# Performance work log

Measured on AMD Instinct MI355X. Metric: run time of the kernel, lower is better.

## Reference

```python
import jax, jax.numpy as jnp
import numpy as np
import math

B, N, DMODEL, H = 8, 1024, 256, 8
HEAD_DIM = DMODEL // H


def setup_inputs() -> dict:
    key = jax.random.key(0)
    ks = jax.random.split(key, 8)
    x = jax.random.normal(ks[0], (B, N, DMODEL), dtype=jnp.float32)
    # symmetric-ish nonnegative pairwise distances
    adj = jax.random.uniform(ks[1], (B, N, N), dtype=jnp.float32) * 10.0
    mask = jax.random.uniform(ks[2], (B, N)) < 0.9  # bool, mostly valid nodes
    W_qkv = jax.random.normal(ks[3], (DMODEL, 3 * DMODEL), dtype=jnp.float32) / math.sqrt(DMODEL)
    b_qkv = jax.random.normal(ks[4], (3 * DMODEL,), dtype=jnp.float32) * 0.01
    shifts = jnp.arange(1.0, H + 1.0, dtype=jnp.float32)  # initial_shifts
    widths = jnp.ones((H,), dtype=jnp.float32)            # initial_widths
    # self_loop_W = 1/head_dim + U(0,1), non-trainable
    self_loop_w = 1.0 / HEAD_DIM + jax.random.uniform(ks[5], (H,), dtype=jnp.float32)
    return {"x": x, "adj": adj, "mask": mask, "W_qkv": W_qkv, "b_qkv": b_qkv,
            "shifts": shifts, "widths": widths, "self_loop_w": self_loop_w}


def reference(x, adj, mask, W_qkv, b_qkv, shifts, widths, self_loop_w):
    b, n, _ = x.shape
    h = shifts.shape[0]
    d = W_qkv.shape[1] // (3 * h)
    qkv = (x @ W_qkv + b_qkv).reshape(b, n, 3, h, d)
    qkv = jnp.transpose(qkv, (2, 0, 3, 1, 4))  # [3, B, H, N, D]
    Q, K, V = qkv[0], qkv[1], qkv[2]
    scores = jnp.einsum('bhnd,bhmd->bhnm', Q, K) / jnp.sqrt(jnp.float32(d))
    # Gaussian moire focus on adjacency distances, per head
    sh = shifts.reshape(1, h, 1, 1)
    w = jnp.maximum(widths, 0.5).reshape(1, h, 1, 1)
    moire = jnp.exp(-((adj[:, None, :, :] - sh) ** 2) / w)
    adjusted = scores + jnp.log(jnp.maximum(moire, 1e-6))
    eye = jnp.eye(n, dtype=adjusted.dtype)  # [N, N]
    adjusted = adjusted + eye * self_loop_w.reshape(1, h, 1, 1)
    mask2d = (mask[:, :, None] & mask[:, None, :])[:, None, :, :]  # [B,1,N,N]
    adjusted = jnp.where(mask2d, adjusted, jnp.float32(-1000000.0))
    attn = jax.nn.softmax(adjusted, axis=-1)
    out = jnp.einsum('bhnm,bhmd->bhnd', attn, V)
    return jnp.transpose(out, (0, 2, 1, 3)).reshape(b, n, h * d)
```

## Files before the change

### kernel.cpp

```cpp
#include <hip/hip_runtime.h>

#define BB 8
#define NN 1024
#define DM 256
#define HH 8
#define HD 32
#define TC 768

typedef __bf16 bf16x8 __attribute__((ext_vector_type(8)));
typedef __bf16 bf16x4 __attribute__((ext_vector_type(4)));
typedef float  f32x4  __attribute__((ext_vector_type(4)));
typedef unsigned int u32;

__global__ __launch_bounds__(256) void precast(
    const float* __restrict__ x, const float* __restrict__ W,
    __bf16* __restrict__ xb, __bf16* __restrict__ Wt)
{
  const int tid = threadIdx.x;
  const int bid = blockIdx.x;
  if (bid < 48) {
    __shared__ __bf16 T[64][65];
    const int ct = bid % 12, kt = bid / 12;
    const int c0 = ct * 64, k0 = kt * 64;
    #pragma unroll
    for (int i = 0; i < 16; ++i) {
      int e = tid + i * 256, kk = e >> 6, cc = e & 63;
      T[cc][kk] = (__bf16)W[(size_t)(k0 + kk) * TC + c0 + cc];
    }
    __syncthreads();
    #pragma unroll
    for (int i = 0; i < 16; ++i) {
      int e = tid + i * 256, cc = e >> 6, kk = e & 63;
      Wt[(size_t)(c0 + cc) * DM + k0 + kk] = T[cc][kk];
    }
  } else {
    const size_t e = (size_t)(bid - 48) * 256 + tid;
    const float4 v = ((const float4*)x)[e];
    bf16x4 o;
    o[0] = (__bf16)v.x; o[1] = (__bf16)v.y;
    o[2] = (__bf16)v.z; o[3] = (__bf16)v.w;
    ((bf16x4*)xb)[e] = o;
  }
}

__global__ __launch_bounds__(256, 3) void qkv_gemm(
    const __bf16* __restrict__ xb, const __bf16* __restrict__ Wt,
    const float* __restrict__ bias, __bf16* __restrict__ Qb,
    __bf16* __restrict__ Kb, __bf16* __restrict__ Vt)
{
  __shared__ __align__(16) char LDSU[49152];
  __bf16* As0 = (__bf16*)LDSU;
  __bf16* Bs0 = (__bf16*)(LDSU + 16384);
  __bf16* As1 = (__bf16*)(LDSU + 24576);
  __bf16* Bs1 = (__bf16*)(LDSU + 40960);

  const int tid  = threadIdx.x;
  const int w    = tid >> 6, lane = tid & 63;
  const int n16  = lane & 15, quad = lane >> 4;
  const int m0   = blockIdx.y * 128, c0 = blockIdx.x * 64;
  const int bb   = m0 >> 10, n0 = m0 & 1023;

  const int stRow = w*8 + (lane >> 3);
  const int stG   = (lane & 7) ^ (lane >> 3);
  const __bf16* gA = &xb[(size_t)(m0 + stRow)*DM + stG*8];
  const __bf16* gB = &Wt[(size_t)(c0 + stRow)*DM + stG*8];

#define QKV_STAGE(Adst, Bdst, K0) do {                                        \
    _Pragma("unroll")                                                         \
    for (int i_ = 0; i_ < 4; ++i_) {                                          \
      const __bf16* gp_ = gA + (size_t)(i_*32)*DM + (K0);                     \
      __bf16* lp_ = (Adst) + (i_*32 + w*8)*64;                                \
      __builtin_amdgcn_global_load_lds(                                       \
          (const __attribute__((address_space(1))) u32*)gp_,                  \
          (__attribute__((address_space(3))) u32*)lp_, 16, 0, 0);             \
    }                                                                         \
    _Pragma("unroll")                                                         \
    for (int i_ = 0; i_ < 2; ++i_) {                                          \
      const __bf16* gp_ = gB + (size_t)(i_*32)*DM + (K0);                     \
      __bf16* lp_ = (Bdst) + (i_*32 + w*8)*64;                                \
      __builtin_amdgcn_global_load_lds(                                       \
          (const __attribute__((address_space(1))) u32*)gp_,                  \
          (__attribute__((address_space(3))) u32*)lp_, 16, 0, 0);             \
    }                                                                         \
  } while (0)

  f32x4 acc[2][4] = {};

  QKV_STAGE(As0, Bs0, 0);
  __syncthreads();

  #pragma unroll
  for (int kk = 0; kk < 4; ++kk) {
    __bf16* Ac = (kk & 1) ? As1 : As0;
    __bf16* Bc = (kk & 1) ? Bs1 : Bs0;
    if (kk == 0)      QKV_STAGE(As1, Bs1, 64);
    else if (kk == 1) QKV_STAGE(As0, Bs0, 128);
    else if (kk == 2) QKV_STAGE(As1, Bs1, 192);
    #pragma unroll
    for (int ks = 0; ks < 2; ++ks) {
      const int ch = ((ks*4 + quad) ^ (n16 & 7)) * 8;
      bf16x8 af0 = *(const bf16x8*)&Ac[(w*32 + n16)*64 + ch];
      bf16x8 af1 = *(const bf16x8*)&Ac[(w*32 + 16 + n16)*64 + ch];
      #pragma unroll
      for (int cb = 0; cb < 4; ++cb) {
        bf16x8 bfb = *(const bf16x8*)&Bc[(cb*16 + n16)*64 + ch];
        acc[0][cb] = __builtin_amdgcn_mfma_f32_16x16x32_bf16(af0, bfb, acc[0][cb], 0, 0, 0);
        acc[1][cb] = __builtin_amdgcn_mfma_f32_16x16x32_bf16(af1, bfb, acc[1][cb], 0, 0, 0);
      }
    }
    __syncthreads();
  }

  float bv[4];
  #pragma unroll
  for (int cb = 0; cb < 4; ++cb) bv[cb] = bias[c0 + cb*16 + n16];

  if (c0 < 512) {
    __bf16* Ct = (__bf16*)LDSU;
    #pragma unroll
    for (int cb = 0; cb < 4; ++cb)
      #pragma unroll
      for (int mb = 0; mb < 2; ++mb)
        #pragma unroll
        for (int r = 0; r < 4; ++r)
          Ct[(w*32 + mb*16 + quad*4 + r)*72 + cb*16 + n16] =
              (__bf16)(acc[mb][cb][r] + bv[cb]);
    __syncthreads();
    const int chunk = tid & 3, hh = (tid >> 2) & 1, rbase = tid >> 3;
    const int c_head = c0 + hh*32;
    const int h = (c_head >> 5) & 7;
    __bf16* base = (c_head >> 8) ? Kb : Qb;
    #pragma unroll
    for (int it = 0; it < 4; ++it) {
      int rl = rbase + it*32;
      bf16x8 v = *(const bf16x8*)&Ct[rl*72 + hh*32 + chunk*8];
      *(bf16x8*)&base[((size_t)((bb*HH + h)*NN + n0 + rl))*HD + chunk*8] = v;
    }
  } else {
    __bf16* CtT = (__bf16*)LDSU;
    #pragma unroll
    for (int cb = 0; cb < 4; ++cb)
      #pragma unroll
      for (int mb = 0; mb < 2; ++mb) {
        bf16x4 t;
        #pragma unroll
        for (int r = 0; r < 4; ++r) t[r] = (__bf16)(acc[mb][cb][r] + bv[cb]);
        *(bf16x4*)&CtT[(cb*16 + n16)*136 + w*32 + mb*16 + quad*4] = t;
      }
    __syncthreads();
    const int col = tid >> 2, sg = tid & 3;
    const int c = c0 + col;
    const int h = (c >> 5) & 7, dd = c & 31;
    __bf16* dst = &Vt[((size_t)((bb*HH + h)*HD + dd))*NN + n0 + sg*32];
    const __bf16* srcp = &CtT[col*136 + sg*32];
    #pragma unroll
    for (int q2 = 0; q2 < 4; ++q2)
      *(bf16x8*)&dst[q2*8] = *(const bf16x8*)&srcp[q2*8];
  }
}

__global__ __launch_bounds__(256, 8) void attn_kernel(
    const __bf16* __restrict__ Q, const __bf16* __restrict__ K,
    const __bf16* __restrict__ Vt, const float* __restrict__ adj,
    const int* __restrict__ mask, const float* __restrict__ shifts,
    const float* __restrict__ widths, const float* __restrict__ slw,
    float* __restrict__ out)
{
  __shared__ __align__(16) __bf16 Ks[2][64][32];
  __shared__ __align__(16) __bf16 Vts[2][32][64];
  __shared__ __align__(16) __bf16 Ps[32][72];

  const int tid  = threadIdx.x;
  const int w    = tid >> 6, lane = tid & 63;
  const int n16  = lane & 15, quad = lane >> 4;
  const int qg   = w >> 1, jh = w & 1;
  const int bh   = blockIdx.x >> 5, qt = blockIdx.x & 31;
  const int b    = bh >> 3, h = bh & 7;
  const int q0   = qt * 32;

  const float L2E   = 1.4426950408889634f;
  const float sh    = shifts[h];
  const float ninvw = -L2E / fmaxf(widths[h], 0.5f);
  const float slv   = slw[h] * L2E;
  const float scl   = 0.17677669529663687f * L2E;
  const float MASKV = -28.0f;
  const float c1 = -2.0f * sh * ninvw;
  const float c2 = sh * sh * ninvw;

  const int srow = tid >> 2, sseg = tid & 3;
  const int vd   = tid >> 3, vsg  = tid & 7;
  const __bf16* Kg = K + (size_t)bh*NN*HD;
  const __bf16* Vg = Vt + (size_t)bh*HD*NN;
  const __bf16* ksrc = Kg + srow*HD + (sseg ^ (srow & 3))*8;
  const __bf16* vsrc = Vg + (size_t)vd*NN + (vsg ^ (vd & 7))*8;
  __bf16* kdst0 = &Ks[0][0][0] + tid*8;
  __bf16* kdst1 = &Ks[1][0][0] + tid*8;
  __bf16* vdst0 = &Vts[0][0][0] + tid*8;
  __bf16* vdst1 = &Vts[1][0][0] + tid*8;

#define GLDS(g, l) __builtin_amdgcn_global_load_lds(                          \
    (const __attribute__((address_space(1))) u32*)(g),                        \
    (__attribute__((address_space(3))) u32*)(l), 16, 0, 0)

  GLDS(ksrc, kdst0);
  GLDS(vsrc, vdst0);

  const bf16x8 qf =
      *(const bf16x8*)&Q[((size_t)bh*NN + q0 + qg*16 + n16)*HD + quad*8];
  int mq[4];
  #pragma unroll
  for (int r = 0; r < 4; ++r) mq[r] = mask[b*NN + q0 + qg*16 + quad*4 + r];

  const float* ar0 = adj + ((size_t)(b*NN + q0 + qg*16 + quad*4))*NN + jh*32 + n16;
  const float* ar1 = ar0 + NN;
  const float* ar2 = ar0 + 2*NN;
  const float* ar3 = ar0 + 3*NN;
  const int*   mrp = mask + b*NN + jh*32 + n16;

  const int kbc = (quad ^ (n16 & 3)) * 8;
  const int vbc = (((jh << 2) + quad) ^ (n16 & 7)) * 8;

  const f32x4 zero = {0.f, 0.f, 0.f, 0.f};
  f32x4 o0 = zero, o1 = zero, lacc = zero;
  bf16x8 onesb;
  #pragma unroll
  for (int i = 0; i < 8; ++i) onesb[i] = (__bf16)1.0f;

  const bool mydiagH = (jh == (qt & 1));
  const int  dT  = qt >> 1;
  const int  dlr = n16 - quad*4;

  __syncthreads();

  #pragma unroll 2
  for (int jtl = 0; jtl < 16; ++jtl) {
    const int cur = jtl & 1;
    const int j0  = jtl * 64;

    if (jtl < 15) {
      const __bf16* kg = ksrc + (size_t)(j0 + 64)*HD;
      const __bf16* vg = vsrc + (j0 + 64);
      if (cur) { GLDS(kg, kdst0); GLDS(vg, vdst0); }
      else     { GLDS(kg, kdst1); GLDS(vg, vdst1); }
    }

    int mj[2];
    #pragma unroll
    for (int cb = 0; cb < 2; ++cb) mj[cb] = mrp[j0 + cb*16];
    float av[4][2];
    #pragma unroll
    for (int cb = 0; cb < 2; ++cb) {
      av[0][cb] = ar0[j0 + cb*16];
      av[1][cb] = ar1[j0 + cb*16];
      av[2][cb] = ar2[j0 + cb*16];
      av[3][cb] = ar3[j0 + cb*16];
    }

    f32x4 s[2];
    #pragma unroll
    for (int cb = 0; cb < 2; ++cb) {
      bf16x8 kf = *(const bf16x8*)&Ks[cur][jh*32 + cb*16 + n16][kbc];
      s[cb] = __builtin_amdgcn_mfma_f32_16x16x32_bf16(qf, kf, zero, 0, 0, 0);
    }
    bf16x8 b0 = *(const bf16x8*)&Vts[cur][n16][vbc];
    bf16x8 b1 = *(const bf16x8*)&Vts[cur][16 + n16][vbc];

    const bool diagt = mydiagH && (jtl == dT);
    #pragma unroll
    for (int r = 0; r < 4; ++r) {
      #pragma unroll
      for (int cb = 0; cb < 2; ++cb) {
        float a   = av[r][cb];
        float mo  = fmaf(a, fmaf(a, ninvw, c1), c2);
        float val = fmaf(s[cb][r], scl, mo);
        if (diagt && (cb == qg) && (dlr == r)) val += slv;
        bool ok = (mq[r] != 0) && (mj[cb] != 0);
        val = ok ? val : MASKV;
        Ps[qg*16 + quad*4 + r][jh*32 + cb*16 + n16] =
            (__bf16)__builtin_amdgcn_exp2f(val);
      }
    }

    bf16x8 a0 = *(const bf16x8*)&Ps[qg*16 + n16][jh*32 + quad*8];
    o0   = __builtin_amdgcn_mfma_f32_16x16x32_bf16(a0, b0, o0, 0, 0, 0);
    o1   = __builtin_amdgcn_mfma_f32_16x16x32_bf16(a0, b1, o1, 0, 0, 0);
    lacc = __builtin_amdgcn_mfma_f32_16x16x32_bf16(a0, onesb, lacc, 0, 0, 0);

    __syncthreads();
  }

  float* red = (float*)&Ks[0][0][0];
  if (jh) {
    float* p = red + (size_t)(qg*64 + lane)*12;
    *(f32x4*)&p[0] = o0; *(f32x4*)&p[4] = o1; *(f32x4*)&p[8] = lacc;
  }
  __syncthreads();
  if (!jh) {
    const float* p = red + (size_t)(qg*64 + lane)*12;
    o0   += *(const f32x4*)&p[0];
    o1   += *(const f32x4*)&p[4];
    lacc += *(const f32x4*)&p[8];
    #pragma unroll
    for (int r = 0; r < 4; ++r) {
      const float invl = 1.0f / lacc[r];
      const int n = q0 + qg*16 + quad*4 + r;
      float* og = out + ((size_t)(b*NN + n))*DM + h*HD;
      og[n16]      = o0[r] * invl;
      og[16 + n16] = o1[r] * invl;
    }
  }
}

extern "C" void kernel_launch(void* const* d_in, const int* in_sizes, int n_in,
                              void* d_out, int out_size, void* d_ws, size_t ws_size,
                              hipStream_t stream) {
  const float* x      = (const float*)d_in[0];
  const float* adj    = (const float*)d_in[1];
  const int*   mask   = (const int*)d_in[2];
  const float* W      = (const float*)d_in[3];
  const float* bias   = (const float*)d_in[4];
  const float* shifts = (const float*)d_in[5];
  const float* widths = (const float*)d_in[6];
  const float* slwp   = (const float*)d_in[7];
  float* out = (float*)d_out;

  const size_t BHND = (size_t)BB*HH*NN*HD;
  const size_t WTN  = (size_t)TC*DM;
  __bf16* xbuf = (__bf16*)d_ws;
  __bf16* Wt   = xbuf + BHND;
  __bf16* Qb   = Wt + WTN;
  __bf16* Kb   = Qb + BHND;
  __bf16* Vt   = Kb + BHND;

  precast<<<dim3(48 + (int)(BHND/4/256)), 256, 0, stream>>>(x, W, xbuf, Wt);
  qkv_gemm<<<dim3(TC/64, (BB*NN)/128), 256, 0, stream>>>(xbuf, Wt, bias, Qb, Kb, Vt);
  attn_kernel<<<dim3(BB*HH*32), 256, 0, stream>>>(Qb, Kb, Vt, adj, mask,
                                                  shifts, widths, slwp, out);
}
```

Baseline: 137.9 us.

## Load K/V fragments directly from global and drop per-tile block barriers

The attention kernel no longer stages K and V tiles through double-buffered LDS with global_load_lds. Each wave now loads its own MFMA fragments straight from global memory, and the probability tile becomes a private per-wave LDS buffer. Together these remove the __syncthreads that ran on every key tile. The cost is redundant K/V global loads across waves, with no explicit prefetch to hide their latency, so it relies on the L2 cache.

```diff
diff --git a/kernel.cpp b/kernel.cpp
--- a/kernel.cpp
+++ b/kernel.cpp
@@ -166,9 +166,8 @@
     const float* __restrict__ widths, const float* __restrict__ slw,
     float* __restrict__ out)
 {
-  __shared__ __align__(16) __bf16 Ks[2][64][32];
-  __shared__ __align__(16) __bf16 Vts[2][32][64];
-  __shared__ __align__(16) __bf16 Ps[32][72];
+  __shared__ __align__(16) __bf16 Ps[4][16][40];
+  __shared__ __align__(16) float  Red[2][64][12];
 
   const int tid  = threadIdx.x;
   const int w    = tid >> 6, lane = tid & 63;
@@ -187,23 +186,12 @@
   const float c1 = -2.0f * sh * ninvw;
   const float c2 = sh * sh * ninvw;
 
-  const int srow = tid >> 2, sseg = tid & 3;
-  const int vd   = tid >> 3, vsg  = tid & 7;
   const __bf16* Kg = K + (size_t)bh*NN*HD;
   const __bf16* Vg = Vt + (size_t)bh*HD*NN;
-  const __bf16* ksrc = Kg + srow*HD + (sseg ^ (srow & 3))*8;
-  const __bf16* vsrc = Vg + (size_t)vd*NN + (vsg ^ (vd & 7))*8;
-  __bf16* kdst0 = &Ks[0][0][0] + tid*8;
-  __bf16* kdst1 = &Ks[1][0][0] + tid*8;
-  __bf16* vdst0 = &Vts[0][0][0] + tid*8;
-  __bf16* vdst1 = &Vts[1][0][0] + tid*8;
-
-#define GLDS(g, l) __builtin_amdgcn_global_load_lds(                          \
-    (const __attribute__((address_space(1))) u32*)(g),                        \
-    (__attribute__((address_space(3))) u32*)(l), 16, 0, 0)
-
-  GLDS(ksrc, kdst0);
-  GLDS(vsrc, vdst0);
+
+  const __bf16* kfp  = Kg + (size_t)(jh*32 + n16)*HD + quad*8;
+  const __bf16* vfp0 = Vg + (size_t)n16*NN + jh*32 + quad*8;
+  const __bf16* vfp1 = vfp0 + (size_t)16*NN;
 
   const bf16x8 qf =
       *(const bf16x8*)&Q[((size_t)bh*NN + q0 + qg*16 + n16)*HD + quad*8];
@@ -217,9 +205,6 @@
   const float* ar3 = ar0 + 3*NN;
   const int*   mrp = mask + b*NN + jh*32 + n16;
 
-  const int kbc = (quad ^ (n16 & 3)) * 8;
-  const int vbc = (((jh << 2) + quad) ^ (n16 & 7)) * 8;
-
   const f32x4 zero = {0.f, 0.f, 0.f, 0.f};
   f32x4 o0 = zero, o1 = zero, lacc = zero;
   bf16x8 onesb;
@@ -230,23 +215,19 @@
   const int  dT  = qt >> 1;
   const int  dlr = n16 - quad*4;
 
-  __syncthreads();
+  __bf16 (*myPs)[40] = Ps[w];
 
   #pragma unroll 2
   for (int jtl = 0; jtl < 16; ++jtl) {
-    const int cur = jtl & 1;
-    const int j0  = jtl * 64;
-
-    if (jtl < 15) {
-      const __bf16* kg = ksrc + (size_t)(j0 + 64)*HD;
-      const __bf16* vg = vsrc + (j0 + 64);
-      if (cur) { GLDS(kg, kdst0); GLDS(vg, vdst0); }
-      else     { GLDS(kg, kdst1); GLDS(vg, vdst1); }
-    }
+    const int j0 = jtl * 64;
+
+    bf16x8 kf0 = *(const bf16x8*)&kfp[(size_t)j0*HD];
+    bf16x8 kf1 = *(const bf16x8*)&kfp[(size_t)(j0 + 16)*HD];
+    bf16x8 b0  = *(const bf16x8*)&vfp0[j0];
+    bf16x8 b1  = *(const bf16x8*)&vfp1[j0];
 
     int mj[2];
-    #pragma unroll
-    for (int cb = 0; cb < 2; ++cb) mj[cb] = mrp[j0 + cb*16];
+    mj[0] = mrp[j0]; mj[1] = mrp[j0 + 16];
     float av[4][2];
     #pragma unroll
     for (int cb = 0; cb < 2; ++cb) {
@@ -256,14 +237,8 @@
       av[3][cb] = ar3[j0 + cb*16];
     }
 
-    f32x4 s[2];
-    #pragma unroll
-    for (int cb = 0; cb < 2; ++cb) {
-      bf16x8 kf = *(const bf16x8*)&Ks[cur][jh*32 + cb*16 + n16][kbc];
-      s[cb] = __builtin_amdgcn_mfma_f32_16x16x32_bf16(qf, kf, zero, 0, 0, 0);
-    }
-    bf16x8 b0 = *(const bf16x8*)&Vts[cur][n16][vbc];
-    bf16x8 b1 = *(const bf16x8*)&Vts[cur][16 + n16][vbc];
+    f32x4 s0 = __builtin_amdgcn_mfma_f32_16x16x32_bf16(qf, kf0, zero, 0, 0, 0);
+    f32x4 s1 = __builtin_amdgcn_mfma_f32_16x16x32_bf16(qf, kf1, zero, 0, 0, 0);
 
     const bool diagt = mydiagH && (jtl == dT);
     #pragma unroll
@@ -272,31 +247,27 @@
       for (int cb = 0; cb < 2; ++cb) {
         float a   = av[r][cb];
         float mo  = fmaf(a, fmaf(a, ninvw, c1), c2);
-        float val = fmaf(s[cb][r], scl, mo);
+        float val = fmaf((cb ? s1[r] : s0[r]), scl, mo);
         if (diagt && (cb == qg) && (dlr == r)) val += slv;
         bool ok = (mq[r] != 0) && (mj[cb] != 0);
         val = ok ? val : MASKV;
-        Ps[qg*16 + quad*4 + r][jh*32 + cb*16 + n16] =
-            (__bf16)__builtin_amdgcn_exp2f(val);
+        myPs[quad*4 + r][cb*16 + n16] = (__bf16)__builtin_amdgcn_exp2f(val);
       }
     }
 
-    bf16x8 a0 = *(const bf16x8*)&Ps[qg*16 + n16][jh*32 + quad*8];
+    bf16x8 a0 = *(const bf16x8*)&myPs[n16][quad*8];
     o0   = __builtin_amdgcn_mfma_f32_16x16x32_bf16(a0, b0, o0, 0, 0, 0);
     o1   = __builtin_amdgcn_mfma_f32_16x16x32_bf16(a0, b1, o1, 0, 0, 0);
     lacc = __builtin_amdgcn_mfma_f32_16x16x32_bf16(a0, onesb, lacc, 0, 0, 0);
-
-    __syncthreads();
-  }
-
-  float* red = (float*)&Ks[0][0][0];
+  }
+
   if (jh) {
-    float* p = red + (size_t)(qg*64 + lane)*12;
+    float* p = &Red[qg][lane][0];
     *(f32x4*)&p[0] = o0; *(f32x4*)&p[4] = o1; *(f32x4*)&p[8] = lacc;
   }
   __syncthreads();
   if (!jh) {
-    const float* p = red + (size_t)(qg*64 + lane)*12;
+    const float* p = &Red[qg][lane][0];
     o0   += *(const f32x4*)&p[0];
     o1   += *(const f32x4*)&p[4];
     lacc += *(const f32x4*)&p[8];
```

After: 179.8 us. 1.3x slower.
